# Kernel optimization log

Measured on AMD Instinct MI355X. Metric: run time of the kernel, lower is better.

## Reference

```python
import jax, jax.numpy as jnp
import numpy as np
from jax import lax

B, CIN, COUT, H, W = 16, 320, 320, 64, 64
R, NUM_LORAS, LORA_STRIDE, SCALE, K = 4, 50, 4, 1.0, 3


def setup_inputs() -> dict:
    key = jax.random.key(0)
    k1, k2, k3, k4, k5, k6 = jax.random.split(key, 6)
    x = jax.random.normal(k1, (B, CIN, H, W), dtype=jnp.float32)
    lora_id = jax.random.randint(k2, (B,), 0, NUM_LORAS * LORA_STRIDE, dtype=jnp.int64)
    conv_w = jax.random.normal(k3, (COUT, CIN, K, K), dtype=jnp.float32) * (1.0 / np.sqrt(CIN * K * K))
    conv_b = jax.random.normal(k4, (COUT,), dtype=jnp.float32) * 0.01
    # stacked LoRA banks: down [L, r, Cin, 3, 3], up [L, Cout, r] (1x1 conv squeezed)
    down_w = jax.random.normal(k5, (NUM_LORAS, R, CIN, K, K), dtype=jnp.float32) * (1.0 / R)
    up_w = jax.random.normal(k6, (NUM_LORAS, COUT, R), dtype=jnp.float32) * 0.02
    return {"x": x, "conv_w": conv_w, "conv_b": conv_b, "down_w": down_w, "up_w": up_w, "lora_id": lora_id}


def _conv3x3(x, w):
    # x: [N, C, H, W], w: [O, C, 3, 3], stride 1, padding 1
    return lax.conv_general_dilated(x, w, (1, 1), [(1, 1), (1, 1)],
                                    dimension_numbers=("NCHW", "OIHW", "NCHW"))


def reference(x, conv_w, conv_b, down_w, up_w, lora_id):
    idx = lora_id // LORA_STRIDE                      # [B]
    active = (idx >= 0).astype(x.dtype)               # [B] mask; negative -> base conv only
    safe = jnp.clip(idx, 0, NUM_LORAS - 1)
    # base conv on full batch (dropout is identity at inference)
    base = _conv3x3(x, conv_w) + conv_b[None, :, None, None]  # [B, Cout, H, W]
    # per-sample gathered down conv (3x3), vmapped over batch (MoE-style dispatch)
    wd = down_w[safe]                                 # [B, r, Cin, 3, 3]
    down = jax.vmap(lambda xi, wi: _conv3x3(xi[None], wi)[0])(x, wd)  # [B, r, H, W]
    # per-sample 1x1 up conv as einsum with gathered up weights
    up = jnp.einsum("brhw,bor->bohw", down, up_w[safe])  # [B, Cout, H, W]
    return base + SCALE * up * active[:, None, None, None]
```

## Files before the change

kernel.cpp:

```cpp
#include <hip/hip_runtime.h>

typedef unsigned short ushort_t;
typedef unsigned int   uint_t;
typedef __attribute__((ext_vector_type(8))) short  short8;
typedef __attribute__((ext_vector_type(4))) float  float4v;
typedef __attribute__((ext_vector_type(4))) uint_t uint4v;

#define B_    16
#define CIN_  320
#define COUT_ 320
#define NLORA 50
#define R_    4

#define XPAD_ELEMS ((size_t)B_ * 66 * 66 * CIN_)
#define WEFF_OFF   (XPAD_ELEMS * 2)

__device__ __forceinline__ ushort_t bf16rne(float f) {
  uint_t u = __float_as_uint(f);
  u = (u + 0x7FFFu + ((u >> 16) & 1u)) >> 16;
  return (ushort_t)u;
}

__device__ __forceinline__ void gld16(const ushort_t* g, ushort_t* l) {
  __builtin_amdgcn_global_load_lds(
      (const __attribute__((address_space(1))) void*)g,
      (__attribute__((address_space(3))) void*)l,
      16, 0, 0);
}

__global__ __launch_bounds__(1024)
void zero_borders(ushort_t* __restrict__ x_pad) {
  const int b = blockIdx.x;
  ushort_t* base = x_pad + (size_t)b * 66 * 66 * CIN_;
  const int tid = threadIdx.x;
  for (int g = tid; g < 2 * 2640; g += 1024) {
    int r = (g >= 2640) ? 1 : 0;
    int off = (g - r * 2640) * 8;
    *(uint4v*)(base + (size_t)(r * 65) * 66 * CIN_ + off) = (uint4v)0u;
  }
  for (int g = tid; g < 64 * 2 * 40; g += 1024) {
    int c8 = g % 40;
    int t2 = g / 40;
    int col = (t2 & 1) * 65;
    int row = 1 + (t2 >> 1);
    *(uint4v*)(base + ((size_t)row * 66 + col) * CIN_ + c8 * 8) = (uint4v)0u;
  }
}

__global__ __launch_bounds__(256)
void pad_convert(const float* __restrict__ x, ushort_t* __restrict__ x_pad) {
  __shared__ float t[64][65];
  const int cc  = blockIdx.x;
  const int h   = blockIdx.y;
  const int b   = blockIdx.z;
  const int tid = threadIdx.x;
  #pragma unroll
  for (int it = 0; it < 16; ++it) {
    int idx = it * 256 + tid;
    int cl = idx >> 6, wl = idx & 63;
    t[cl][wl] = x[(((size_t)(b * CIN_ + cc * 64 + cl)) * 64 + h) * 64 + wl];
  }
  __syncthreads();
  #pragma unroll
  for (int it = 0; it < 8; ++it) {
    int flat = (it * 256 + tid) * 2;
    int wl = flat >> 6, cl = flat & 63;
    uint_t u0 = bf16rne(t[cl][wl]);
    uint_t u1 = bf16rne(t[cl + 1][wl]);
    *(uint_t*)(x_pad + (((size_t)(b * 66 + h + 1)) * 66 + (wl + 1)) * CIN_ + cc * 64 + cl)
        = u0 | (u1 << 16);
  }
}

__global__ __launch_bounds__(320)
void merge_weights(const float* __restrict__ conv_w, const float* __restrict__ down_w,
                   const float* __restrict__ up_w,  const void* __restrict__ lora,
                   ushort_t* __restrict__ W_eff) {
  const int o = blockIdx.x;
  const int b = blockIdx.y;
  const int c = threadIdx.x;

  const int* p32 = (const int*)lora;
  bool odd0 = true;
  #pragma unroll
  for (int i = 1; i < 16; i += 2) odd0 = odd0 && (p32[i] == 0);
  long long raw = odd0 ? ((const long long*)lora)[b] : (long long)p32[b];
  long long idx = (raw >= 0) ? (raw >> 2) : -(((-raw) + 3) >> 2);
  float act = (idx >= 0) ? 1.0f : 0.0f;
  int l = (int)(idx < 0 ? 0 : (idx > (NLORA - 1) ? (NLORA - 1) : idx));

  float up[R_];
  #pragma unroll
  for (int r = 0; r < R_; ++r)
    up[r] = up_w[((size_t)l * COUT_ + o) * R_ + r] * act;

  #pragma unroll
  for (int tap = 0; tap < 9; ++tap) {
    float v = conv_w[((size_t)o * CIN_ + c) * 9 + tap];
    #pragma unroll
    for (int r = 0; r < R_; ++r)
      v += up[r] * down_w[(((size_t)l * R_ + r) * CIN_ + c) * 9 + tap];
    W_eff[(((size_t)b * 9 + tap) * COUT_ + o) * CIN_ + c] = bf16rne(v);
  }
}

#define XS_GRAN_PAD 2688
#define WT_GRAN     2304
#define BUF_BYTES   ((XS_GRAN_PAD + WT_GRAN) * 16)

__global__ __launch_bounds__(512, 2)
void conv_main(const ushort_t* __restrict__ x_pad, const ushort_t* __restrict__ W_eff,
               const float* __restrict__ conv_b, float* __restrict__ out) {
  __shared__ __align__(16) char smem[2 * BUF_BYTES];

  const int tid = threadIdx.x;
  const int lin = blockIdx.x;
  const int wg  = (lin & 7) * 80 + (lin >> 3);
  const int b   = wg / 40;
  const int rem = wg - b * 40;
  const int o0  = (rem >> 3) * 64;
  const int h0  = (rem & 7) * 8;

  const int wv = tid >> 6;
  const int la = tid & 15;
  const int q  = (tid >> 4) & 3;

  int xsrc[6];
  #pragma unroll
  for (int i = 0; i < 6; ++i) {
    int g = i * 512 + tid;
    if (g > 2639) g = 2639;
    int qq = g & 3, t = g >> 2;
    int hh = t / 66, ww = t - hh * 66;
    xsrc[i] = ((b * 66 + h0 + hh) * 66 + ww) * CIN_ + ((qq ^ (ww & 3)) * 8);
  }
  int wsrc[5];
  #pragma unroll
  for (int j = 0; j < 5; ++j) {
    int g = j * 512 + tid;
    if (g > 2303) g = 2303;
    int qq = g & 3, o = (g >> 2) & 63, tap = g >> 8;
    wsrc[j] = ((b * 9 + tap) * COUT_ + o0 + o) * CIN_ + ((qq ^ (o & 3)) * 8);
  }

  float4v acc[4][4];
  #pragma unroll
  for (int i = 0; i < 4; ++i)
    #pragma unroll
    for (int n = 0; n < 4; ++n) acc[i][n] = (float4v)0.0f;

  auto STAGE = [&](int sel, int c0) {
    ushort_t* xb = (ushort_t*)(smem + sel * BUF_BYTES);
    ushort_t* wb = xb + XS_GRAN_PAD * 8;
    #pragma unroll
    for (int i = 0; i < 5; ++i)
      gld16(x_pad + xsrc[i] + c0, xb + (i * 512 + wv * 64) * 8);
    if (wv < 2)
      gld16(x_pad + xsrc[5] + c0, xb + (5 * 512 + wv * 64) * 8);
    #pragma unroll
    for (int j = 0; j < 4; ++j)
      gld16(W_eff + wsrc[j] + c0, wb + (j * 512 + wv * 64) * 8);
    if (wv < 4)
      gld16(W_eff + wsrc[4] + c0, wb + (4 * 512 + wv * 64) * 8);
  };

  STAGE(0, 0);
  int cur = 0;
  for (int t = 0; t < 10; ++t) {
    asm volatile("" ::: "memory");
    __builtin_amdgcn_s_barrier();
    asm volatile("" ::: "memory");
    if (t < 9) STAGE(cur ^ 1, (t + 1) * 32);
    __builtin_amdgcn_sched_barrier(0);
    if (t < 9) asm volatile("s_waitcnt vmcnt(9)" ::: "memory");
    else       asm volatile("s_waitcnt vmcnt(0)" ::: "memory");
    __builtin_amdgcn_sched_barrier(0);
    __builtin_amdgcn_s_barrier();
    asm volatile("" ::: "memory");

    const ushort_t* xb = (const ushort_t*)(smem + cur * BUF_BYTES);
    const ushort_t* wb = xb + XS_GRAN_PAD * 8;
    #pragma unroll
    for (int tap = 0; tap < 9; ++tap) {
      const int kh = tap / 3, kw = tap - kh * 3;
      short8 bf[4];
      #pragma unroll
      for (int n = 0; n < 4; ++n) {
        int o = n * 16 + la;
        bf[n] = *(const short8*)(wb + ((tap * 64 + o) * 4 + (q ^ (o & 3))) * 8);
      }
      const int hh = wv + kh;
      #pragma unroll
      for (int i = 0; i < 4; ++i) {
        int ww = i * 16 + la + kw;
        short8 af = *(const short8*)(xb + ((hh * 66 + ww) * 4 + (q ^ (ww & 3))) * 8);
        #pragma unroll
        for (int n = 0; n < 4; ++n)
          acc[i][n] = __builtin_amdgcn_mfma_f32_16x16x32_bf16(af, bf[n], acc[i][n], 0, 0, 0);
      }
    }
    cur ^= 1;
  }

  float* lc = (float*)smem;
  #pragma unroll
  for (int half = 0; half < 2; ++half) {
    __syncthreads();
    #pragma unroll
    for (int nn = 0; nn < 2; ++nn) {
      const int nsub  = half * 2 + nn;
      const int n_loc = nn * 16 + la;
      #pragma unroll
      for (int i = 0; i < 4; ++i) {
        const int m = wv * 64 + i * 16 + q * 4;
        *(float4v*)(lc + n_loc * 516 + m) = acc[i][nsub];
      }
    }
    __syncthreads();
    for (int f = tid; f < 32 * 128; f += 512) {
      int n_loc = f >> 7;
      int m4 = (f & 127) * 4;
      int o = o0 + half * 32 + n_loc;
      float4v v = *(const float4v*)(lc + n_loc * 516 + m4);
      v += conv_b[o];
      *(float4v*)(out + ((size_t)(b * COUT_ + o) * 4096) + h0 * 64 + m4) = v;
    }
  }
}

extern "C" void kernel_launch(void* const* d_in, const int* in_sizes, int n_in,
                              void* d_out, int out_size, void* d_ws, size_t ws_size,
                              hipStream_t stream) {
  const float* x      = (const float*)d_in[0];
  const float* conv_w = (const float*)d_in[1];
  const float* conv_b = (const float*)d_in[2];
  const float* down_w = (const float*)d_in[3];
  const float* up_w   = (const float*)d_in[4];
  const void*  lora   = d_in[5];
  float* out = (float*)d_out;

  ushort_t* x_pad = (ushort_t*)d_ws;
  ushort_t* W_eff = (ushort_t*)((char*)d_ws + WEFF_OFF);

  zero_borders <<<dim3(16),        1024, 0, stream>>>(x_pad);
  pad_convert  <<<dim3(5, 64, 16), 256,  0, stream>>>(x, x_pad);
  merge_weights<<<dim3(320, 16),   320,  0, stream>>>(conv_w, down_w, up_w, lora, W_eff);
  conv_main    <<<dim3(640),       512,  0, stream>>>(x_pad, W_eff, conv_b, out);
}
```

Baseline: 305.0 us.

## Chunk channel layout, shrink conv tiles to 8x32x32, fold border zeroing

Changes x_pad and W_eff to channel-chunked layouts of 32 channels per chunk, so each pipeline stage loads contiguous blocks and advances a pointer instead of recomputing offsets, and drops the XOR swizzle. Shrinks the conv output tile from 8x64 pixels by 64 channels to 8x32 by 32 channels, giving 2560 workgroups at 4 per CU with less LDS and fewer accumulators. Removes the separate border-zeroing kernel by doing it inside pad_convert. Smaller tiles mean more re-reading of halo and weights and fewer MFMAs per LDS load, and the unswizzled LDS reads may hit bank conflicts.

```diff
diff --git a/kernel.cpp b/kernel.cpp
--- a/kernel.cpp
+++ b/kernel.cpp
@@ -11,8 +11,11 @@
 #define COUT_ 320
 #define NLORA 50
 #define R_    4
-
-#define XPAD_ELEMS ((size_t)B_ * 66 * 66 * CIN_)
+#define NCH   10
+
+#define XCHUNK (66*66*32)
+#define WCHUNK (9*COUT_*32)
+#define XPAD_ELEMS ((size_t)B_ * NCH * XCHUNK)
 #define WEFF_OFF   (XPAD_ELEMS * 2)
 
 __device__ __forceinline__ ushort_t bf16rne(float f) {
@@ -26,25 +29,6 @@
       (const __attribute__((address_space(1))) void*)g,
       (__attribute__((address_space(3))) void*)l,
       16, 0, 0);
-}
-
-__global__ __launch_bounds__(1024)
-void zero_borders(ushort_t* __restrict__ x_pad) {
-  const int b = blockIdx.x;
-  ushort_t* base = x_pad + (size_t)b * 66 * 66 * CIN_;
-  const int tid = threadIdx.x;
-  for (int g = tid; g < 2 * 2640; g += 1024) {
-    int r = (g >= 2640) ? 1 : 0;
-    int off = (g - r * 2640) * 8;
-    *(uint4v*)(base + (size_t)(r * 65) * 66 * CIN_ + off) = (uint4v)0u;
-  }
-  for (int g = tid; g < 64 * 2 * 40; g += 1024) {
-    int c8 = g % 40;
-    int t2 = g / 40;
-    int col = (t2 & 1) * 65;
-    int row = 1 + (t2 >> 1);
-    *(uint4v*)(base + ((size_t)row * 66 + col) * CIN_ + c8 * 8) = (uint4v)0u;
-  }
 }
 
 __global__ __launch_bounds__(256)
@@ -67,8 +51,27 @@
     int wl = flat >> 6, cl = flat & 63;
     uint_t u0 = bf16rne(t[cl][wl]);
     uint_t u1 = bf16rne(t[cl + 1][wl]);
-    *(uint_t*)(x_pad + (((size_t)(b * 66 + h + 1)) * 66 + (wl + 1)) * CIN_ + cc * 64 + cl)
-        = u0 | (u1 << 16);
+    int chunk = cc * 2 + (cl >> 5);
+    *(uint_t*)(x_pad + (((size_t)(b * NCH + chunk) * 66 + (h + 1)) * 66 + (wl + 1)) * 32
+               + (cl & 31)) = u0 | (u1 << 16);
+  }
+  if (h == 0) {
+    #pragma unroll
+    for (int s = 0; s < 2; ++s) {
+      ushort_t* base = x_pad + (size_t)(b * NCH + cc * 2 + s) * XCHUNK;
+      for (int g = tid; g < 528; g += 256) {
+        int r = (g >= 264) ? 1 : 0;
+        int g2 = g - r * 264;
+        int col = g2 >> 2, qg = g2 & 3;
+        *(uint4v*)(base + ((size_t)(r * 65) * 66 + col) * 32 + qg * 8) = (uint4v)0u;
+      }
+      for (int g = tid; g < 512; g += 256) {
+        int row = 1 + (g >> 3);
+        int col = ((g >> 2) & 1) * 65;
+        int qg  = g & 3;
+        *(uint4v*)(base + ((size_t)row * 66 + col) * 32 + qg * 8) = (uint4v)0u;
+      }
+    }
   }
 }
 
@@ -94,137 +97,129 @@
   for (int r = 0; r < R_; ++r)
     up[r] = up_w[((size_t)l * COUT_ + o) * R_ + r] * act;
 
+  const size_t wb = (size_t)(b * NCH + (c >> 5)) * 9;
   #pragma unroll
   for (int tap = 0; tap < 9; ++tap) {
     float v = conv_w[((size_t)o * CIN_ + c) * 9 + tap];
     #pragma unroll
     for (int r = 0; r < R_; ++r)
       v += up[r] * down_w[(((size_t)l * R_ + r) * CIN_ + c) * 9 + tap];
-    W_eff[(((size_t)b * 9 + tap) * COUT_ + o) * CIN_ + c] = bf16rne(v);
-  }
-}
-
-#define XS_GRAN_PAD 2688
-#define WT_GRAN     2304
-#define BUF_BYTES   ((XS_GRAN_PAD + WT_GRAN) * 16)
-
-__global__ __launch_bounds__(512, 2)
+    W_eff[((wb + tap) * COUT_ + o) * 32 + (c & 31)] = bf16rne(v);
+  }
+}
+
+#define XG    1360
+#define XGP   1408
+#define WG    1152
+#define TOTG  2560
+#define BUF_B (TOTG * 16)
+
+__global__ __launch_bounds__(512, 4)
 void conv_main(const ushort_t* __restrict__ x_pad, const ushort_t* __restrict__ W_eff,
                const float* __restrict__ conv_b, float* __restrict__ out) {
-  __shared__ __align__(16) char smem[2 * BUF_BYTES];
+  __shared__ __align__(16) char smem[2 * BUF_B];
 
   const int tid = threadIdx.x;
   const int lin = blockIdx.x;
-  const int wg  = (lin & 7) * 80 + (lin >> 3);
-  const int b   = wg / 40;
-  const int rem = wg - b * 40;
-  const int o0  = (rem >> 3) * 64;
-  const int h0  = (rem & 7) * 8;
+  const int wg  = (lin & 7) * 320 + (lin >> 3);
+  const int b   = wg / 160;
+  const int rem = wg - b * 160;
+  const int o0  = (rem >> 4) * 32;
+  const int hw  = rem & 15;
+  const int h0  = (hw & 7) * 8;
+  const int w0  = (hw >> 3) * 32;
 
   const int wv = tid >> 6;
   const int la = tid & 15;
   const int q  = (tid >> 4) & 3;
 
-  int xsrc[6];
-  #pragma unroll
-  for (int i = 0; i < 6; ++i) {
-    int g = i * 512 + tid;
-    if (g > 2639) g = 2639;
-    int qq = g & 3, t = g >> 2;
-    int hh = t / 66, ww = t - hh * 66;
-    xsrc[i] = ((b * 66 + h0 + hh) * 66 + ww) * CIN_ + ((qq ^ (ww & 3)) * 8);
-  }
-  int wsrc[5];
-  #pragma unroll
-  for (int j = 0; j < 5; ++j) {
-    int g = j * 512 + tid;
-    if (g > 2303) g = 2303;
-    int qq = g & 3, o = (g >> 2) & 63, tap = g >> 8;
-    wsrc[j] = ((b * 9 + tap) * COUT_ + o0 + o) * CIN_ + ((qq ^ (o & 3)) * 8);
-  }
-
-  float4v acc[4][4];
-  #pragma unroll
-  for (int i = 0; i < 4; ++i)
-    #pragma unroll
-    for (int n = 0; n < 4; ++n) acc[i][n] = (float4v)0.0f;
-
-  auto STAGE = [&](int sel, int c0) {
-    ushort_t* xb = (ushort_t*)(smem + sel * BUF_BYTES);
-    ushort_t* wb = xb + XS_GRAN_PAD * 8;
-    #pragma unroll
-    for (int i = 0; i < 5; ++i)
-      gld16(x_pad + xsrc[i] + c0, xb + (i * 512 + wv * 64) * 8);
-    if (wv < 2)
-      gld16(x_pad + xsrc[5] + c0, xb + (5 * 512 + wv * 64) * 8);
-    #pragma unroll
-    for (int j = 0; j < 4; ++j)
-      gld16(W_eff + wsrc[j] + c0, wb + (j * 512 + wv * 64) * 8);
-    if (wv < 4)
-      gld16(W_eff + wsrc[4] + c0, wb + (4 * 512 + wv * 64) * 8);
+  const ushort_t* psrc[5];
+  int step[5];
+  #pragma unroll
+  for (int r = 0; r < 5; ++r) {
+    int g = r * 512 + tid;
+    if (g < XGP) {
+      int gx = (g < XG) ? g : (XG - 1);
+      int qq = gx & 3, t = gx >> 2;
+      int hh = t / 34, ww = t - hh * 34;
+      psrc[r] = x_pad + (size_t)b * NCH * XCHUNK
+              + (((h0 + hh) * 66 + (w0 + ww)) * 32 + qq * 8);
+      step[r] = XCHUNK;
+    } else {
+      int gw = g - XGP;
+      int qq = gw & 3, t2 = gw >> 2;
+      int o = t2 & 31, tap = t2 >> 5;
+      psrc[r] = W_eff + (size_t)b * NCH * WCHUNK
+              + ((tap * COUT_ + o0 + o) * 32 + qq * 8);
+      step[r] = WCHUNK;
+    }
+  }
+
+  float4v acc[2][2];
+  #pragma unroll
+  for (int i = 0; i < 2; ++i)
+    #pragma unroll
+    for (int n = 0; n < 2; ++n) acc[i][n] = (float4v)0.0f;
+
+  auto STAGE = [&](int sel) {
+    ushort_t* bufb = (ushort_t*)(smem + sel * BUF_B);
+    #pragma unroll
+    for (int r = 0; r < 5; ++r) {
+      gld16(psrc[r], bufb + (r * 512 + wv * 64) * 8);
+      psrc[r] += step[r];
+    }
   };
 
-  STAGE(0, 0);
+  STAGE(0);
   int cur = 0;
-  for (int t = 0; t < 10; ++t) {
+  for (int t = 0; t < NCH; ++t) {
     asm volatile("" ::: "memory");
     __builtin_amdgcn_s_barrier();
     asm volatile("" ::: "memory");
-    if (t < 9) STAGE(cur ^ 1, (t + 1) * 32);
+    if (t < NCH - 1) STAGE(cur ^ 1);
     __builtin_amdgcn_sched_barrier(0);
-    if (t < 9) asm volatile("s_waitcnt vmcnt(9)" ::: "memory");
-    else       asm volatile("s_waitcnt vmcnt(0)" ::: "memory");
+    if (t < NCH - 1) asm volatile("s_waitcnt vmcnt(5)" ::: "memory");
+    else             asm volatile("s_waitcnt vmcnt(0)" ::: "memory");
     __builtin_amdgcn_sched_barrier(0);
     __builtin_amdgcn_s_barrier();
     asm volatile("" ::: "memory");
 
-    const ushort_t* xb = (const ushort_t*)(smem + cur * BUF_BYTES);
-    const ushort_t* wb = xb + XS_GRAN_PAD * 8;
+    const ushort_t* xb = (const ushort_t*)(smem + cur * BUF_B);
+    const ushort_t* wb = xb + XGP * 8;
     #pragma unroll
     for (int tap = 0; tap < 9; ++tap) {
       const int kh = tap / 3, kw = tap - kh * 3;
-      short8 bf[4];
-      #pragma unroll
-      for (int n = 0; n < 4; ++n) {
-        int o = n * 16 + la;
-        bf[n] = *(const short8*)(wb + ((tap * 64 + o) * 4 + (q ^ (o & 3))) * 8);
-      }
+      short8 bf0 = *(const short8*)(wb + ((tap * 32 +      la) * 4 + q) * 8);
+      short8 bf1 = *(const short8*)(wb + ((tap * 32 + 16 + la) * 4 + q) * 8);
       const int hh = wv + kh;
       #pragma unroll
-      for (int i = 0; i < 4; ++i) {
-        int ww = i * 16 + la + kw;
-        short8 af = *(const short8*)(xb + ((hh * 66 + ww) * 4 + (q ^ (ww & 3))) * 8);
-        #pragma unroll
-        for (int n = 0; n < 4; ++n)
-          acc[i][n] = __builtin_amdgcn_mfma_f32_16x16x32_bf16(af, bf[n], acc[i][n], 0, 0, 0);
+      for (int i = 0; i < 2; ++i) {
+        short8 af = *(const short8*)(xb + ((hh * 34 + i * 16 + la + kw) * 4 + q) * 8);
+        acc[i][0] = __builtin_amdgcn_mfma_f32_16x16x32_bf16(af, bf0, acc[i][0], 0, 0, 0);
+        acc[i][1] = __builtin_amdgcn_mfma_f32_16x16x32_bf16(af, bf1, acc[i][1], 0, 0, 0);
       }
     }
     cur ^= 1;
   }
 
+  __syncthreads();
   float* lc = (float*)smem;
   #pragma unroll
-  for (int half = 0; half < 2; ++half) {
-    __syncthreads();
-    #pragma unroll
-    for (int nn = 0; nn < 2; ++nn) {
-      const int nsub  = half * 2 + nn;
-      const int n_loc = nn * 16 + la;
-      #pragma unroll
-      for (int i = 0; i < 4; ++i) {
-        const int m = wv * 64 + i * 16 + q * 4;
-        *(float4v*)(lc + n_loc * 516 + m) = acc[i][nsub];
-      }
-    }
-    __syncthreads();
-    for (int f = tid; f < 32 * 128; f += 512) {
-      int n_loc = f >> 7;
-      int m4 = (f & 127) * 4;
-      int o = o0 + half * 32 + n_loc;
-      float4v v = *(const float4v*)(lc + n_loc * 516 + m4);
-      v += conv_b[o];
-      *(float4v*)(out + ((size_t)(b * COUT_ + o) * 4096) + h0 * 64 + m4) = v;
-    }
+  for (int n = 0; n < 2; ++n) {
+    const int n_loc = n * 16 + la;
+    #pragma unroll
+    for (int i = 0; i < 2; ++i)
+      *(float4v*)(lc + n_loc * 260 + wv * 32 + i * 16 + q * 4) = acc[i][n];
+  }
+  __syncthreads();
+  const size_t ob = ((size_t)(b * COUT_ + o0)) * 4096 + h0 * 64 + w0;
+  for (int f = tid; f < 32 * 64; f += 512) {
+    int n_loc = f >> 6;
+    int m4 = (f & 63) * 4;
+    int row = m4 >> 5, col = m4 & 31;
+    float4v v = *(const float4v*)(lc + n_loc * 260 + m4);
+    v += conv_b[o0 + n_loc];
+    *(float4v*)(out + ob + (size_t)n_loc * 4096 + row * 64 + col) = v;
   }
 }
 
@@ -242,8 +237,7 @@
   ushort_t* x_pad = (ushort_t*)d_ws;
   ushort_t* W_eff = (ushort_t*)((char*)d_ws + WEFF_OFF);
 
-  zero_borders <<<dim3(16),        1024, 0, stream>>>(x_pad);
-  pad_convert  <<<dim3(5, 64, 16), 256,  0, stream>>>(x, x_pad);
-  merge_weights<<<dim3(320, 16),   320,  0, stream>>>(conv_w, down_w, up_w, lora, W_eff);
-  conv_main    <<<dim3(640),       512,  0, stream>>>(x_pad, W_eff, conv_b, out);
-}
+  pad_convert  <<<dim3(5, 64, 16), 256, 0, stream>>>(x, x_pad);
+  merge_weights<<<dim3(320, 16),   320, 0, stream>>>(conv_w, down_w, up_w, lora, W_eff);
+  conv_main    <<<dim3(2560),      512, 0, stream>>>(x_pad, W_eff, conv_b, out);
+}
```

After: 295.5 us. 1.03x faster.
